# Performance work log

Measured on AMD Instinct MI355X. Metric: run time of the kernel, lower is better.

Reference implementation:

```python
import jax, jax.numpy as jnp
import numpy as np


def _conv_same(x, w):
    # NHWC input, HWIO kernel, stride 1, SAME padding
    return jax.lax.conv_general_dilated(
        x, w, window_strides=(1, 1), padding='SAME',
        dimension_numbers=('NHWC', 'HWIO', 'NHWC'))


def _maxpool2(x):
    return jax.lax.reduce_window(
        x, -jnp.inf, jax.lax.max,
        window_dimensions=(1, 2, 2, 1), window_strides=(1, 2, 2, 1),
        padding='VALID')


def _binarize(x):
    # sign binarization with straight-through estimator (XNOR-net / Riptide)
    return x + jax.lax.stop_gradient(jnp.sign(x) - x)


def _binary_conv_relu(x, w):
    # BinaryConv2D: binarize activations and weights, conv, relu, no bias
    return jax.nn.relu(_conv_same(_binarize(x), _binarize(w)))


def setup_inputs() -> dict:
    key = jax.random.key(0)
    ks = jax.random.split(key, 32)
    d = {}
    d['x'] = jax.random.normal(ks[0], (128, 32, 32, 3), dtype=jnp.float32)
    d['w1'] = jax.random.normal(ks[1], (3, 3, 3, 128), dtype=jnp.float32) * 0.1
    d['b1'] = jax.random.normal(ks[2], (128,), dtype=jnp.float32) * 0.1
    chans = [128, 128, 256, 256, 512, 512]
    kshapes = [(3, 3, 128, 128), (3, 3, 128, 256), (3, 3, 256, 256),
               (3, 3, 256, 512), (3, 3, 512, 512)]
    for i, shp in zip(range(2, 7), kshapes):
        d[f'w{i}'] = jax.random.normal(ks[2 + i], shp, dtype=jnp.float32) * 0.1
    for i in range(1, 7):
        c = chans[i - 1]
        d[f'bn{i}_scale'] = jax.random.uniform(ks[10 + i], (c,), dtype=jnp.float32, minval=0.5, maxval=1.5)
        d[f'bn{i}_bias'] = jax.random.normal(ks[20 + i], (c,), dtype=jnp.float32) * 0.1
    d['dense_w'] = jax.random.normal(ks[30], (512, 10), dtype=jnp.float32) * 0.05
    d['dense_b'] = jax.random.normal(ks[31], (10,), dtype=jnp.float32) * 0.05
    return d


def reference(x, w1, b1, bn1_scale, bn1_bias, w2, bn2_scale, bn2_bias,
              w3, bn3_scale, bn3_bias, w4, bn4_scale, bn4_bias,
              w5, bn5_scale, bn5_bias, w6, bn6_scale, bn6_bias,
              dense_w, dense_b):
    # conv1: normal float conv + relu, then BN (inference: fused scale/bias)
    h = jax.nn.relu(_conv_same(x, w1) + b1)
    h = h * bn1_scale + bn1_bias
    # conv2 (binary) -> pool -> bn2
    h = _binary_conv_relu(h, w2)
    h = _maxpool2(h)
    h = h * bn2_scale + bn2_bias
    # conv3 (binary) -> bn3
    h = _binary_conv_relu(h, w3)
    h = h * bn3_scale + bn3_bias
    # conv4 (binary) -> pool -> bn4
    h = _binary_conv_relu(h, w4)
    h = _maxpool2(h)
    h = h * bn4_scale + bn4_bias
    # conv5 (binary) -> bn5
    h = _binary_conv_relu(h, w5)
    h = h * bn5_scale + bn5_bias
    # conv6 (binary) -> pool -> bn6
    h = _binary_conv_relu(h, w6)
    h = _maxpool2(h)  # -> [B, 4, 4, 512]
    h = h * bn6_scale + bn6_bias
    # Dense applied on last axis (original code has no flatten): [B,4,4,10]
    logits = jnp.einsum('bhwc,cd->bhwd', h, dense_w) + dense_b
    return jax.nn.softmax(logits, axis=-1)
```

## Files before the change

kernel.cpp:

```cpp
#include <hip/hip_runtime.h>
#include <cstdint>

typedef unsigned long long u64;

__device__ __forceinline__ int pc_acc(u64 a, u64 w, int acc) {
    u64 x = a ^ w;
    acc = __builtin_popcount((unsigned)x) + acc;
    acc = __builtin_popcount((unsigned)(x >> 32)) + acc;
    return acc;
}

__global__ __launch_bounds__(256) void prep_kernel(
        const float* __restrict__ w2, const float* __restrict__ w3,
        const float* __restrict__ w4, const float* __restrict__ w5,
        const float* __restrict__ w6,
        u64* __restrict__ wp2, u64* __restrict__ wp3, u64* __restrict__ wp4,
        u64* __restrict__ wp5, u64* __restrict__ wp6,
        u64* __restrict__ pz, int nz) {
    const int ZB = 1024;
    if (blockIdx.x < ZB) {
        int i = blockIdx.x * 256 + threadIdx.x;
        const int stride = ZB * 256;
        for (; i < nz; i += stride) pz[i] = 0;
        return;
    }
    int wid = ((blockIdx.x - ZB) * 256 + threadIdx.x) >> 6;
    int lane = threadIdx.x & 63;
    const float* w; u64* wp; int Wi, Cout, base;
    if      (wid <  2304) { w = w2; wp = wp2; Wi = 2; Cout = 128; base = 0; }
    else if (wid <  6912) { w = w3; wp = wp3; Wi = 2; Cout = 256; base = 2304; }
    else if (wid < 16128) { w = w4; wp = wp4; Wi = 4; Cout = 256; base = 6912; }
    else if (wid < 34560) { w = w5; wp = wp5; Wi = 4; Cout = 512; base = 16128; }
    else if (wid < 71424) { w = w6; wp = wp6; Wi = 8; Cout = 512; base = 34560; }
    else return;
    int id = wid - base;
    int oc = id % Cout;
    int tw = id / Cout;
    int tap = tw / Wi, cw = tw % Wi;
    int Cin = Wi * 64;
    float v = w[((size_t)tap * Cin + cw * 64 + lane) * Cout + oc];
    u64 mask = __ballot(!(v > 0.0f));
    if (lane == 0) wp[(size_t)oc * (9 * Wi) + tap * Wi + cw] = mask;
}

__global__ __launch_bounds__(128) void conv1_pack_kernel(
        const float* __restrict__ x, const float* __restrict__ w1,
        const float* __restrict__ b1, const float* __restrict__ s1,
        const float* __restrict__ bb1, u64* __restrict__ p1) {
    const int t = threadIdx.x;
    const int oc = t;
    const int bx = blockIdx.x;
    const int xseg = (bx & 3) << 3;
    const int y = (bx >> 2) & 31;
    const int b = bx >> 7;

    double wreg[27];
    #pragma unroll
    for (int k = 0; k < 27; k++) wreg[k] = (double)w1[k * 128 + oc];
    const double b1v = (double)b1[oc];
    const double tneg = -(double)bb1[oc] / (double)s1[oc];
    const bool always = tneg < 0.0;
    const double thr = tneg - b1v;

    double acc[8];
    #pragma unroll
    for (int i = 0; i < 8; i++) acc[i] = 0.0;

    #pragma unroll
    for (int ky = 0; ky < 3; ky++) {
        int iy = y - 1 + ky;
        if (iy < 0 || iy > 31) continue;
        #pragma unroll
        for (int col = 0; col < 10; col++) {
            int ix = xseg - 1 + col;
            if (ix < 0 || ix > 31) continue;
            const float* xp = x + ((b * 32 + iy) * 32 + ix) * 3;
            #pragma unroll
            for (int c = 0; c < 3; c++) {
                double xv = (double)xp[c];
                #pragma unroll
                for (int kx = 0; kx < 3; kx++) {
                    int px = col - kx;
                    if (px >= 0 && px < 8)
                        acc[px] += xv * wreg[(ky * 3 + kx) * 3 + c];
                }
            }
        }
    }
    #pragma unroll
    for (int px = 0; px < 8; px++) {
        bool bit = always || (acc[px] > thr);
        u64 m = __ballot(bit);
        if ((t & 63) == 0)
            p1[((size_t)(b * 34 + y + 1) * 34 + xseg + px + 1) * 2 + (t >> 6)] = m;
    }
}

template<int WI, int H, int W, int COUT, bool POOL, int XS, bool BITOUT>
__global__ __launch_bounds__(256, 4) void bconv4_kernel(
        const u64* __restrict__ in, const u64* __restrict__ wp,
        const float* __restrict__ bns, const float* __restrict__ bnb,
        u64* __restrict__ outb, float* __restrict__ outf) {
    constexpr int ROWS = POOL ? 2 : 1;
    constexpr int Ho   = POOL ? H / 2 : H;
    constexpr int Wo   = POOL ? W / 2 : W;
    constexpr int WoW  = COUT >> 6;
    constexpr int Hp   = H + 2, Wp = W + 2;
    constexpr int Wg   = W / XS;
    constexpr int Wog  = Wo / XS;
    constexpr int CH   = (WI < 4) ? WI : 4;
    constexpr int NC   = WI / CH;

    const int lane = threadIdx.x & 63;
    int wid = (blockIdx.x * blockDim.x + threadIdx.x) >> 6;
    wid = __builtin_amdgcn_readfirstlane(wid);
    const int wordo = wid % WoW;
    int t = wid / WoW;
    const int xg = t % XS; t /= XS;
    const int oy = t % Ho;
    const int b  = t / Ho;
    if (b >= 128) return;
    const int oc = wordo * 64 + lane;
    const int c0 = xg * Wg;
    const int base = POOL ? oy * 2 : oy;

    int m[ROWS][Wg];
    #pragma unroll
    for (int r = 0; r < ROWS; r++)
        #pragma unroll
        for (int c = 0; c < Wg; c++) m[r][c] = 0;

    int S_top = 0, S_bot = 0, S_lef = 0, S_rig = 0;
    int C_tl = 0, C_tr = 0, C_bl = 0, C_br = 0;

    const u64* wlane = wp + (size_t)oc * (9 * WI);
    const u64* inb = in + (((size_t)b * Hp + base) * Wp + c0) * WI;

    #pragma unroll 1
    for (int kc = 0; kc < 3 * NC; kc++) {
        const int ky = kc / NC;
        const int ch = kc % NC;
        const u64* wptr = wlane + ky * 3 * WI + ch * CH;
        u64 wk[3][CH];
        #pragma unroll
        for (int kx = 0; kx < 3; kx++)
            #pragma unroll
            for (int cw = 0; cw < CH; cw++)
                wk[kx][cw] = wptr[kx * WI + cw];

        int pg[3];
        #pragma unroll
        for (int kx = 0; kx < 3; kx++) {
            int s = 0;
            #pragma unroll
            for (int cw = 0; cw < CH; cw++) s += (int)__popcll(wk[kx][cw]);
            pg[kx] = 64 * CH - s;
        }
        S_lef += pg[0]; S_rig += pg[2];
        if (ky == 0) { S_top += pg[0] + pg[1] + pg[2]; C_tl += pg[0]; C_tr += pg[2]; }
        if (ky == 2) { S_bot += pg[0] + pg[1] + pg[2]; C_bl += pg[0]; C_br += pg[2]; }

        #pragma unroll
        for (int r = 0; r < ROWS; r++) {
            const u64* inrow = inb + (size_t)(r + ky) * Wp * WI + ch * CH;
            #pragma unroll
            for (int c = 0; c < Wg + 2; c++) {
                u64 av[CH];
                #pragma unroll
                for (int cw = 0; cw < CH; cw++) av[cw] = inrow[(size_t)c * WI + cw];
                #pragma unroll
                for (int kx = 0; kx < 3; kx++) {
                    const int col = c - kx;
                    if (col < 0 || col >= Wg) continue;
                    int acc = m[r][col];
                    #pragma unroll
                    for (int cw = 0; cw < CH; cw++)
                        acc = pc_acc(av[cw], wk[kx][cw], acc);
                    m[r][col] = acc;
                }
            }
        }
    }

    const double sc = (double)bns[oc];
    const double bi = (double)bnb[oc];

    #pragma unroll
    for (int po = 0; po < Wog; po++) {
        int pmax = 0;
        #pragma unroll
        for (int r = 0; r < ROWS; r++) {
            #pragma unroll
            for (int wx = 0; wx < (POOL ? 2 : 1); wx++) {
                const int lc = POOL ? po * 2 + wx : po;
                const int pc = c0 + lc;
                const int pr = base + r;
                const int top = (pr == 0), bot = (pr == H - 1);
                const int lef = (pc == 0), rig = (pc == W - 1);
                int n_oob = 3 * (top + bot + lef + rig)
                          - (top & lef) - (top & rig) - (bot & lef) - (bot & rig);
                int S = top * S_top + bot * S_bot + lef * S_lef + rig * S_rig
                      - (top & lef) * C_tl - (top & rig) * C_tr
                      - (bot & lef) * C_bl - (bot & rig) * C_br;
                int d = 2 * m[r][lc] + 2 * S - 64 * WI * (9 + n_oob);
                pmax = d > pmax ? d : pmax;
            }
        }
        double h = (double)pmax * sc + bi;
        if constexpr (BITOUT) {
            u64 mask = __ballot(h > 0.0);
            if (lane == 0)
                outb[((size_t)(b * (Ho + 2) + oy + 1) * (Wo + 2) + xg * Wog + po + 1) * WoW + wordo] = mask;
        } else {
            outf[((size_t)(b * Ho + oy) * Wo + xg * Wog + po) * COUT + oc] = (float)h;
        }
    }
}

__global__ __launch_bounds__(256) void dense_softmax_kernel(
        const float* __restrict__ h6, const float* __restrict__ dw,
        const float* __restrict__ db, float* __restrict__ out) {
    int lane = threadIdx.x & 63;
    int r = (blockIdx.x * blockDim.x + threadIdx.x) >> 6;
    if (r >= 2048) return;
    const float* hr = h6 + (size_t)r * 512;
    float part[10];
    #pragma unroll
    for (int d = 0; d < 10; d++) part[d] = 0.f;
    #pragma unroll
    for (int k = 0; k < 8; k++) {
        int c = lane + 64 * k;
        float hv = hr[c];
        const float* dwr = dw + c * 10;
        #pragma unroll
        for (int d = 0; d < 10; d++) part[d] += hv * dwr[d];
    }
    #pragma unroll
    for (int off = 32; off >= 1; off >>= 1) {
        #pragma unroll
        for (int d = 0; d < 10; d++) part[d] += __shfl_down(part[d], off, 64);
    }
    if (lane == 0) {
        float logits[10];
        float mx = -1e30f;
        #pragma unroll
        for (int d = 0; d < 10; d++) { logits[d] = part[d] + db[d]; mx = fmaxf(mx, logits[d]); }
        float se = 0.f;
        #pragma unroll
        for (int d = 0; d < 10; d++) { logits[d] = expf(logits[d] - mx); se += logits[d]; }
        float inv = 1.f / se;
        #pragma unroll
        for (int d = 0; d < 10; d++) out[(size_t)r * 10 + d] = logits[d] * inv;
    }
}

extern "C" void kernel_launch(void* const* d_in, const int* in_sizes, int n_in,
                              void* d_out, int out_size, void* d_ws, size_t ws_size,
                              hipStream_t stream) {
    const float* x    = (const float*)d_in[0];
    const float* w1   = (const float*)d_in[1];
    const float* b1   = (const float*)d_in[2];
    const float* w2   = (const float*)d_in[3];
    const float* w3   = (const float*)d_in[4];
    const float* w4   = (const float*)d_in[5];
    const float* w5   = (const float*)d_in[6];
    const float* w6   = (const float*)d_in[7];
    const float* bn1s = (const float*)d_in[8];
    const float* bn1b = (const float*)d_in[9];
    const float* bn2s = (const float*)d_in[10];
    const float* bn2b = (const float*)d_in[11];
    const float* bn3s = (const float*)d_in[12];
    const float* bn3b = (const float*)d_in[13];
    const float* bn4s = (const float*)d_in[14];
    const float* bn4b = (const float*)d_in[15];
    const float* bn5s = (const float*)d_in[16];
    const float* bn5b = (const float*)d_in[17];
    const float* bn6s = (const float*)d_in[18];
    const float* bn6b = (const float*)d_in[19];
    const float* dw   = (const float*)d_in[20];
    const float* db   = (const float*)d_in[21];
    float* out = (float*)d_out;

    u64* ws  = (u64*)d_ws;
    u64* wp2 = ws;
    u64* wp3 = wp2 + 2304;
    u64* wp4 = wp3 + 4608;
    u64* wp5 = wp4 + 9216;
    u64* wp6 = wp5 + 18432;
    u64* p1  = wp6 + 36864;
    u64* p2  = p1 + 295936;
    u64* p3  = p2 + 82944;
    u64* p4  = p3 + 165888;
    u64* p5  = p4 + 51200;
    float* h6 = (float*)(p5 + 102400);
    const int NPAD = 295936 + 82944 + 165888 + 51200 + 102400;

    prep_kernel<<<1024 + 17856, 256, 0, stream>>>(
        w2, w3, w4, w5, w6, wp2, wp3, wp4, wp5, wp6, p1, NPAD);

    conv1_pack_kernel<<<128*32*4, 128, 0, stream>>>(x, w1, b1, bn1s, bn1b, p1);

    bconv4_kernel<2,32,32,128,true, 2,true ><<<2048, 256, 0, stream>>>(p1, wp2, bn2s, bn2b, p2, nullptr);
    bconv4_kernel<2,16,16,256,false,1,true ><<<2048, 256, 0, stream>>>(p2, wp3, bn3s, bn3b, p3, nullptr);
    bconv4_kernel<4,16,16,256,true, 2,true ><<<2048, 256, 0, stream>>>(p3, wp4, bn4s, bn4b, p4, nullptr);
    bconv4_kernel<4,8,8,512,false,1,true ><<<2048, 256, 0, stream>>>(p4, wp5, bn5s, bn5b, p5, nullptr);
    bconv4_kernel<8,8,8,512,true, 2,false><<<2048, 256, 0, stream>>>(p5, wp6, bn6s, bn6b, nullptr, h6);

    dense_softmax_kernel<<<2048*64/256, 256, 0, stream>>>(h6, dw, db, out);
}
```

Baseline: 364.2 us.

## Remap binary convs so lanes own pixels and iterate over output channels

Replaces the binary conv kernel so each wavefront lane handles one pixel of an 8x8 tile and holds its 3x3 activation neighbourhood in registers. The kernel then loops over a group of output channels, loading weights as wave-uniform (scalar) values. Per-tap weight counts used for the padding correction are now precomputed in the prep kernel instead of recomputed per wave. Pooling uses lane shuffles, and output bits are packed per lane and written as 16, 32 or 64-bit stores. This trades the old per-lane-channel layout, which needed per-lane weight loads, for more register pressure and a serial loop over channels.

```diff
diff --git a/kernel.cpp b/kernel.cpp
--- a/kernel.cpp
+++ b/kernel.cpp
@@ -2,13 +2,6 @@
 #include <cstdint>
 
 typedef unsigned long long u64;
-
-__device__ __forceinline__ int pc_acc(u64 a, u64 w, int acc) {
-    u64 x = a ^ w;
-    acc = __builtin_popcount((unsigned)x) + acc;
-    acc = __builtin_popcount((unsigned)(x >> 32)) + acc;
-    return acc;
-}
 
 __global__ __launch_bounds__(256) void prep_kernel(
         const float* __restrict__ w2, const float* __restrict__ w3,
@@ -16,6 +9,7 @@
         const float* __restrict__ w6,
         u64* __restrict__ wp2, u64* __restrict__ wp3, u64* __restrict__ wp4,
         u64* __restrict__ wp5, u64* __restrict__ wp6,
+        int* __restrict__ corr,
         u64* __restrict__ pz, int nz) {
     const int ZB = 1024;
     if (blockIdx.x < ZB) {
@@ -26,21 +20,40 @@
     }
     int wid = ((blockIdx.x - ZB) * 256 + threadIdx.x) >> 6;
     int lane = threadIdx.x & 63;
-    const float* w; u64* wp; int Wi, Cout, base;
-    if      (wid <  2304) { w = w2; wp = wp2; Wi = 2; Cout = 128; base = 0; }
-    else if (wid <  6912) { w = w3; wp = wp3; Wi = 2; Cout = 256; base = 2304; }
-    else if (wid < 16128) { w = w4; wp = wp4; Wi = 4; Cout = 256; base = 6912; }
-    else if (wid < 34560) { w = w5; wp = wp5; Wi = 4; Cout = 512; base = 16128; }
-    else if (wid < 71424) { w = w6; wp = wp6; Wi = 8; Cout = 512; base = 34560; }
-    else return;
-    int id = wid - base;
-    int oc = id % Cout;
-    int tw = id / Cout;
-    int tap = tw / Wi, cw = tw % Wi;
-    int Cin = Wi * 64;
-    float v = w[((size_t)tap * Cin + cw * 64 + lane) * Cout + oc];
-    u64 mask = __ballot(!(v > 0.0f));
-    if (lane == 0) wp[(size_t)oc * (9 * Wi) + tap * Wi + cw] = mask;
+    if (wid < 71424) {
+        const float* w; u64* wp; int Wi, Cout, base;
+        if      (wid <  2304) { w = w2; wp = wp2; Wi = 2; Cout = 128; base = 0; }
+        else if (wid <  6912) { w = w3; wp = wp3; Wi = 2; Cout = 256; base = 2304; }
+        else if (wid < 16128) { w = w4; wp = wp4; Wi = 4; Cout = 256; base = 6912; }
+        else if (wid < 34560) { w = w5; wp = wp5; Wi = 4; Cout = 512; base = 16128; }
+        else                  { w = w6; wp = wp6; Wi = 8; Cout = 512; base = 34560; }
+        int id = wid - base;
+        int oc = id % Cout;
+        int tw = id / Cout;
+        int tap = tw / Wi, cw = tw % Wi;
+        int Cin = Wi * 64;
+        float v = w[((size_t)tap * Cin + cw * 64 + lane) * Cout + oc];
+        u64 mask = __ballot(!(v > 0.0f));
+        if (lane == 0) wp[(size_t)oc * (9 * Wi) + tap * Wi + cw] = mask;
+    } else if (wid < 71424 + 14976) {
+        int id2 = wid - 71424;
+        const float* w; int Wi, Cout, cbase, lo;
+        if      (id2 <  1152) { w = w2; Wi = 2; Cout = 128; cbase = 0;     lo = 0; }
+        else if (id2 <  3456) { w = w3; Wi = 2; Cout = 256; cbase = 1152;  lo = 1152; }
+        else if (id2 <  5760) { w = w4; Wi = 4; Cout = 256; cbase = 3456;  lo = 3456; }
+        else if (id2 < 10368) { w = w5; Wi = 4; Cout = 512; cbase = 5760;  lo = 5760; }
+        else                  { w = w6; Wi = 8; Cout = 512; cbase = 10368; lo = 10368; }
+        int lid = id2 - lo;
+        int tap = lid % 9;
+        int oc  = lid / 9;
+        int Cin = Wi * 64;
+        int cnt = 0;
+        for (int cw = 0; cw < Wi; cw++) {
+            float v = w[((size_t)tap * Cin + cw * 64 + lane) * Cout + oc];
+            cnt += (int)__popcll(__ballot(v > 0.0f));
+        }
+        if (lane == 0) corr[cbase + oc * 9 + tap] = cnt;
+    }
 }
 
 __global__ __launch_bounds__(128) void conv1_pack_kernel(
@@ -96,123 +109,109 @@
     }
 }
 
-template<int WI, int H, int W, int COUT, bool POOL, int XS, bool BITOUT>
-__global__ __launch_bounds__(256, 4) void bconv4_kernel(
+template<int WI, int H, int W, int COUT, bool POOL, int OCG, bool BITOUT>
+__global__ __launch_bounds__(256, (WI == 8) ? 2 : 4) void bconv5_kernel(
         const u64* __restrict__ in, const u64* __restrict__ wp,
+        const int* __restrict__ corr,
         const float* __restrict__ bns, const float* __restrict__ bnb,
         u64* __restrict__ outb, float* __restrict__ outf) {
-    constexpr int ROWS = POOL ? 2 : 1;
-    constexpr int Ho   = POOL ? H / 2 : H;
-    constexpr int Wo   = POOL ? W / 2 : W;
-    constexpr int WoW  = COUT >> 6;
-    constexpr int Hp   = H + 2, Wp = W + 2;
-    constexpr int Wg   = W / XS;
-    constexpr int Wog  = Wo / XS;
-    constexpr int CH   = (WI < 4) ? WI : 4;
-    constexpr int NC   = WI / CH;
+    constexpr int Hp = H + 2, Wp = W + 2;
+    constexpr int Ho = POOL ? H / 2 : H;
+    constexpr int Wo = POOL ? W / 2 : W;
+    constexpr int WoW = COUT >> 6;
+    constexpr int TY = H / 8, TX = W / 8;
+    constexpr int NG = COUT / OCG;
 
     const int lane = threadIdx.x & 63;
     int wid = (blockIdx.x * blockDim.x + threadIdx.x) >> 6;
     wid = __builtin_amdgcn_readfirstlane(wid);
-    const int wordo = wid % WoW;
-    int t = wid / WoW;
-    const int xg = t % XS; t /= XS;
-    const int oy = t % Ho;
-    const int b  = t / Ho;
+    const int g = wid % NG;
+    int t2 = wid / NG;
+    const int tile = t2 % (TY * TX);
+    const int b = t2 / (TY * TX);
     if (b >= 128) return;
-    const int oc = wordo * 64 + lane;
-    const int c0 = xg * Wg;
-    const int base = POOL ? oy * 2 : oy;
-
-    int m[ROWS][Wg];
-    #pragma unroll
-    for (int r = 0; r < ROWS; r++)
-        #pragma unroll
-        for (int c = 0; c < Wg; c++) m[r][c] = 0;
-
-    int S_top = 0, S_bot = 0, S_lef = 0, S_rig = 0;
-    int C_tl = 0, C_tr = 0, C_bl = 0, C_br = 0;
-
-    const u64* wlane = wp + (size_t)oc * (9 * WI);
-    const u64* inb = in + (((size_t)b * Hp + base) * Wp + c0) * WI;
-
-    #pragma unroll 1
-    for (int kc = 0; kc < 3 * NC; kc++) {
-        const int ky = kc / NC;
-        const int ch = kc % NC;
-        const u64* wptr = wlane + ky * 3 * WI + ch * CH;
-        u64 wk[3][CH];
+    const int ty0 = (tile / TX) * 8, tx0 = (tile % TX) * 8;
+    const int ly = lane >> 3, lx = lane & 7;
+    const int py = ty0 + ly, px = tx0 + lx;
+
+    u64 act[9 * WI];
+    const u64* ib = in + (((size_t)b * Hp + py) * Wp + px) * WI;
+    #pragma unroll
+    for (int ky = 0; ky < 3; ky++)
         #pragma unroll
         for (int kx = 0; kx < 3; kx++)
             #pragma unroll
-            for (int cw = 0; cw < CH; cw++)
-                wk[kx][cw] = wptr[kx * WI + cw];
-
-        int pg[3];
-        #pragma unroll
-        for (int kx = 0; kx < 3; kx++) {
-            int s = 0;
+            for (int cw = 0; cw < WI; cw++)
+                act[(ky * 3 + kx) * WI + cw] = ib[((size_t)ky * Wp + kx) * WI + cw];
+
+    const int ft = (py == 0), fb = (py == H - 1);
+    const int fl = (px == 0), fr = (px == W - 1);
+    const int ctl = ft & fl, ctr = ft & fr, cbl = fb & fl, cbr = fb & fr;
+    const int n_oob = 3 * (ft + fb + fl + fr) - ctl - ctr - cbl - cbr;
+    const int dbase = -64 * WI * (9 + n_oob);
+
+    const int oc0 = g * OCG;
+    const bool master = POOL ? (((ly | lx) & 1) == 0) : true;
+    const int opy = POOL ? (py >> 1) : py, opx = POOL ? (px >> 1) : px;
+
+    u64 mask = 0;
+    #pragma unroll 1
+    for (int o = 0; o < OCG; o++) {
+        const int oc = oc0 + o;
+        const u64* wl = wp + (size_t)oc * (9 * WI);
+        const int* cp = corr + oc * 9;
+
+        int a0 = 0, a1 = 0, a2 = 0, a3 = 0;
+        #pragma unroll
+        for (int ky = 0; ky < 3; ky++) {
+            u64 wv[3 * WI];
             #pragma unroll
-            for (int cw = 0; cw < CH; cw++) s += (int)__popcll(wk[kx][cw]);
-            pg[kx] = 64 * CH - s;
-        }
-        S_lef += pg[0]; S_rig += pg[2];
-        if (ky == 0) { S_top += pg[0] + pg[1] + pg[2]; C_tl += pg[0]; C_tr += pg[2]; }
-        if (ky == 2) { S_bot += pg[0] + pg[1] + pg[2]; C_bl += pg[0]; C_br += pg[2]; }
-
-        #pragma unroll
-        for (int r = 0; r < ROWS; r++) {
-            const u64* inrow = inb + (size_t)(r + ky) * Wp * WI + ch * CH;
+            for (int k = 0; k < 3 * WI; k++) wv[k] = wl[ky * 3 * WI + k];
             #pragma unroll
-            for (int c = 0; c < Wg + 2; c++) {
-                u64 av[CH];
+            for (int kx = 0; kx < 3; kx++)
                 #pragma unroll
-                for (int cw = 0; cw < CH; cw++) av[cw] = inrow[(size_t)c * WI + cw];
-                #pragma unroll
-                for (int kx = 0; kx < 3; kx++) {
-                    const int col = c - kx;
-                    if (col < 0 || col >= Wg) continue;
-                    int acc = m[r][col];
-                    #pragma unroll
-                    for (int cw = 0; cw < CH; cw++)
-                        acc = pc_acc(av[cw], wk[kx][cw], acc);
-                    m[r][col] = acc;
+                for (int cw = 0; cw < WI; cw++) {
+                    u64 xo = act[(ky * 3 + kx) * WI + cw] ^ wv[kx * WI + cw];
+                    const int ai = (kx * WI + cw) & 3;
+                    int lo = __builtin_popcount((unsigned)xo);
+                    int hi = __builtin_popcount((unsigned)(xo >> 32));
+                    if (ai == 0) { a0 = lo + a0; a0 = hi + a0; }
+                    else if (ai == 1) { a1 = lo + a1; a1 = hi + a1; }
+                    else if (ai == 2) { a2 = lo + a2; a2 = hi + a2; }
+                    else { a3 = lo + a3; a3 = hi + a3; }
                 }
-            }
-        }
-    }
-
-    const double sc = (double)bns[oc];
-    const double bi = (double)bnb[oc];
-
-    #pragma unroll
-    for (int po = 0; po < Wog; po++) {
-        int pmax = 0;
-        #pragma unroll
-        for (int r = 0; r < ROWS; r++) {
-            #pragma unroll
-            for (int wx = 0; wx < (POOL ? 2 : 1); wx++) {
-                const int lc = POOL ? po * 2 + wx : po;
-                const int pc = c0 + lc;
-                const int pr = base + r;
-                const int top = (pr == 0), bot = (pr == H - 1);
-                const int lef = (pc == 0), rig = (pc == W - 1);
-                int n_oob = 3 * (top + bot + lef + rig)
-                          - (top & lef) - (top & rig) - (bot & lef) - (bot & rig);
-                int S = top * S_top + bot * S_bot + lef * S_lef + rig * S_rig
-                      - (top & lef) * C_tl - (top & rig) * C_tr
-                      - (bot & lef) * C_bl - (bot & rig) * C_br;
-                int d = 2 * m[r][lc] + 2 * S - 64 * WI * (9 + n_oob);
-                pmax = d > pmax ? d : pmax;
-            }
-        }
-        double h = (double)pmax * sc + bi;
+        }
+        const int m = (a0 + a1) + (a2 + a3);
+
+        const int p0 = cp[0], p1_ = cp[1], p2 = cp[2], p3 = cp[3], p5 = cp[5],
+                  p6 = cp[6], p7 = cp[7], p8 = cp[8];
+        const int A = p0 + p1_ + p2, B = p6 + p7 + p8;
+        const int C = p0 + p3 + p6, D = p2 + p5 + p8;
+        int S = ft * A + fb * B + fl * C + fr * D
+              - ctl * p0 - ctr * p2 - cbl * p6 - cbr * p8;
+        int d = 2 * (m + S) + dbase;
+
+        if constexpr (POOL) {
+            int dm = max(d, __shfl_xor(d, 1, 64));
+            d = max(dm, __shfl_xor(dm, 8, 64));
+        }
+        const int pmax = d > 0 ? d : 0;
+        const double h = (double)pmax * (double)bns[oc] + (double)bnb[oc];
         if constexpr (BITOUT) {
-            u64 mask = __ballot(h > 0.0);
-            if (lane == 0)
-                outb[((size_t)(b * (Ho + 2) + oy + 1) * (Wo + 2) + xg * Wog + po + 1) * WoW + wordo] = mask;
+            mask |= (u64)(h > 0.0) << o;
         } else {
-            outf[((size_t)(b * Ho + oy) * Wo + xg * Wog + po) * COUT + oc] = (float)h;
+            if (master)
+                outf[((size_t)(b * Ho + opy) * Wo + opx) * COUT + oc] = (float)h;
+        }
+    }
+
+    if constexpr (BITOUT) {
+        if (master) {
+            size_t pix = (size_t)(b * (Ho + 2) + opy + 1) * (Wo + 2) + opx + 1;
+            char* bp = (char*)(outb + pix * WoW) + (oc0 >> 3);
+            if constexpr (OCG == 64) *(u64*)bp = mask;
+            else if constexpr (OCG == 32) *(unsigned*)bp = (unsigned)mask;
+            else *(unsigned short*)bp = (unsigned short)mask;
         }
     }
 }
@@ -281,30 +280,37 @@
     const float* db   = (const float*)d_in[21];
     float* out = (float*)d_out;
 
-    u64* ws  = (u64*)d_ws;
-    u64* wp2 = ws;
-    u64* wp3 = wp2 + 2304;
-    u64* wp4 = wp3 + 4608;
-    u64* wp5 = wp4 + 9216;
-    u64* wp6 = wp5 + 18432;
-    u64* p1  = wp6 + 36864;
-    u64* p2  = p1 + 295936;
-    u64* p3  = p2 + 82944;
-    u64* p4  = p3 + 165888;
-    u64* p5  = p4 + 51200;
+    u64* ws   = (u64*)d_ws;
+    u64* wp2  = ws;
+    u64* wp3  = wp2 + 2304;
+    u64* wp4  = wp3 + 4608;
+    u64* wp5  = wp4 + 9216;
+    u64* wp6  = wp5 + 18432;
+    int* corr = (int*)(wp6 + 36864);
+    u64* p1   = wp6 + 36864 + 7488;
+    u64* p2   = p1 + 295936;
+    u64* p3   = p2 + 82944;
+    u64* p4   = p3 + 165888;
+    u64* p5   = p4 + 51200;
     float* h6 = (float*)(p5 + 102400);
     const int NPAD = 295936 + 82944 + 165888 + 51200 + 102400;
 
-    prep_kernel<<<1024 + 17856, 256, 0, stream>>>(
-        w2, w3, w4, w5, w6, wp2, wp3, wp4, wp5, wp6, p1, NPAD);
+    int* c2 = corr + 0;
+    int* c3 = corr + 1152;
+    int* c4 = corr + 3456;
+    int* c5 = corr + 5760;
+    int* c6 = corr + 10368;
+
+    prep_kernel<<<1024 + 21600, 256, 0, stream>>>(
+        w2, w3, w4, w5, w6, wp2, wp3, wp4, wp5, wp6, corr, p1, NPAD);
 
     conv1_pack_kernel<<<128*32*4, 128, 0, stream>>>(x, w1, b1, bn1s, bn1b, p1);
 
-    bconv4_kernel<2,32,32,128,true, 2,true ><<<2048, 256, 0, stream>>>(p1, wp2, bn2s, bn2b, p2, nullptr);
-    bconv4_kernel<2,16,16,256,false,1,true ><<<2048, 256, 0, stream>>>(p2, wp3, bn3s, bn3b, p3, nullptr);
-    bconv4_kernel<4,16,16,256,true, 2,true ><<<2048, 256, 0, stream>>>(p3, wp4, bn4s, bn4b, p4, nullptr);
-    bconv4_kernel<4,8,8,512,false,1,true ><<<2048, 256, 0, stream>>>(p4, wp5, bn5s, bn5b, p5, nullptr);
-    bconv4_kernel<8,8,8,512,true, 2,false><<<2048, 256, 0, stream>>>(p5, wp6, bn6s, bn6b, nullptr, h6);
-
-    dense_softmax_kernel<<<2048*64/256, 256, 0, stream>>>(h6, dw, db, out);
-}
+    bconv5_kernel<2,32,32,128,true, 64,true ><<<1024, 256, 0, stream>>>(p1, wp2, c2, bn2s, bn2b, p2, nullptr);
+    bconv5_kernel<2,16,16,256,false,32,true ><<<1024, 256, 0, stream>>>(p2, wp3, c3, bn3s, bn3b, p3, nullptr);
+    bconv5_kernel<4,16,16,256,true, 32,true ><<<1024, 256, 0, stream>>>(p3, wp4, c4, bn4s, bn4b, p4, nullptr);
+    bconv5_kernel<4,8,8,  512,false,16,true ><<<1024, 256, 0, stream>>>(p4, wp5, c5, bn5s, bn5b, p5, nullptr);
+    bconv5_kernel<8,8,8,  512,true, 16,false><<<1024, 256, 0, stream>>>(p5, wp6, c6, bn6s, bn6b, nullptr, h6);
+
+    dense_softmax_kernel<<<512, 256, 0, stream>>>(h6, dw, db, out);
+}
```

Result: slower. 414.5 us (+13.8%).
